# Optimization experiments

Measured on AMD Instinct MI355X. Metric: run time of the kernel, lower is better.

## Reference

```python
import jax, jax.numpy as jnp
import numpy as np

EMBED = 256
HID = EMBED * 4
NUM_EXPERTS = 4
WINDOW = 16
B, T = 4, 4096
EPS = 1e-5


def _ln(x, g, b):
    m = jnp.mean(x, axis=-1, keepdims=True)
    v = jnp.mean(jnp.square(x - m), axis=-1, keepdims=True)
    return (x - m) / jnp.sqrt(v + EPS) * g + b


def setup_inputs() -> dict:
    key = jax.random.key(0)
    ks = jax.random.split(key, 16)
    s = 0.02
    d = {
        'x': jax.random.normal(ks[0], (B, T, EMBED), jnp.float32),
        'ln1_g': jnp.ones((EMBED,), jnp.float32),
        'ln1_b': jnp.zeros((EMBED,), jnp.float32),
        'qkv_w': jax.random.normal(ks[1], (EMBED, 3 * EMBED), jnp.float32) * s,
        'qkv_b': jnp.zeros((3 * EMBED,), jnp.float32),
        'proj_w': jax.random.normal(ks[2], (EMBED, EMBED), jnp.float32) * s,
        'proj_b': jnp.zeros((EMBED,), jnp.float32),
        'attn_gate': jnp.ones((EMBED,), jnp.float32),
        'ln2_g': jnp.ones((EMBED,), jnp.float32),
        'ln2_b': jnp.zeros((EMBED,), jnp.float32),
        'gating_w': jax.random.normal(ks[3], (EMBED, NUM_EXPERTS), jnp.float32) * s,
        'gating_b': jnp.zeros((NUM_EXPERTS,), jnp.float32),
        'e_w1': jax.random.normal(ks[4], (NUM_EXPERTS, EMBED, HID), jnp.float32) * s,
        'e_b1': jnp.zeros((NUM_EXPERTS, HID), jnp.float32),
        'e_w2': jax.random.normal(ks[5], (NUM_EXPERTS, HID, EMBED), jnp.float32) * s,
        'e_b2': jnp.zeros((NUM_EXPERTS, EMBED), jnp.float32),
    }
    return d


def reference(x, ln1_g, ln1_b, qkv_w, qkv_b, proj_w, proj_b, attn_gate,
              ln2_g, ln2_b, gating_w, gating_b, e_w1, e_b1, e_w2, e_b2):
    Bx, Tx, C = x.shape
    # --- sparse attention branch ---
    h = _ln(x, ln1_g, ln1_b)
    qkv = h @ qkv_w + qkv_b                      # [B,T,3C]
    q, k, v = jnp.split(qkv, 3, axis=-1)
    scores = jnp.einsum('btc,bsc->bts', q, k) / jnp.sqrt(jnp.float32(C))
    idx = jnp.arange(Tx)
    diff = idx[:, None] - idx[None, :]           # i - j
    in_window = (diff >= 0) & (diff <= WINDOW)
    # faithful to torch code: scores outside the window (but causal) stay 0,
    # positions above the diagonal become -inf; softmax over full row
    scores = jnp.where(in_window, scores, 0.0)
    scores = jnp.where(diff >= 0, scores, -jnp.inf)
    att = jax.nn.softmax(scores, axis=-1)        # [B,T,T]
    a_out = jnp.einsum('bts,bsc->btc', att, v) * attn_gate
    x = x + a_out @ proj_w + proj_b
    # --- dense all-expert MoE branch ---
    h2 = _ln(x, ln2_g, ln2_b)
    gates = jax.nn.softmax(h2 @ gating_w + gating_b, axis=-1)     # [B,T,E]
    hid = jax.nn.gelu(jnp.einsum('btc,ech->bteh', h2, e_w1) + e_b1,
                      approximate=False)                           # [B,T,E,H]
    eo = jnp.einsum('bteh,eho->bteo', hid, e_w2) + e_b2            # [B,T,E,C]
    moe_out = jnp.einsum('bte,bteo->bto', gates, eo)
    return x + moe_out
```

## Files before the change

kernel.cpp:

```cpp
#include <hip/hip_runtime.h>
#include <hip/hip_bf16.h>
#include <math.h>

#define T_   4096
#define B_   4
#define C_   256
#define C3_  768
#define H_   1024
#define E_   4
#define M_   (B_*T_)
#define NCH_ 64
#define CHL_ (T_/NCH_)
#define KH_  4096

typedef __attribute__((ext_vector_type(8))) short short8;
typedef __attribute__((ext_vector_type(4))) float floatx4;

__device__ __forceinline__ float b2f(unsigned short u) {
  union { unsigned int i; float f; } x; x.i = ((unsigned int)u) << 16; return x.f;
}
__device__ __forceinline__ unsigned short f2b(float f) {
  __hip_bfloat16 h = __float2bfloat16(f);
  return *reinterpret_cast<unsigned short*>(&h);
}
__device__ __forceinline__ void unpack8(uint4 a, float* f) {
  unsigned int w[4] = {a.x, a.y, a.z, a.w};
  #pragma unroll
  for (int i = 0; i < 4; i++) {
    union { unsigned int u; float g; } lo, hi;
    lo.u = w[i] << 16; hi.u = w[i] & 0xffff0000u;
    f[2*i] = lo.g; f[2*i+1] = hi.g;
  }
}
__device__ __forceinline__ void gl_lds16(const void* g, void* l) {
  __builtin_amdgcn_global_load_lds(
      (const __attribute__((address_space(1))) void*)g,
      (__attribute__((address_space(3))) void*)l, 16, 0, 0);
}
__device__ __forceinline__ float gelu_s(float v) {
  float e = __expf(-1.702f * v);
  return v * __builtin_amdgcn_rcpf(1.0f + e);
}
__device__ __forceinline__ unsigned int pk_fp8x4(float a, float b, float c, float d) {
  unsigned int v = 0;
  v = __builtin_amdgcn_cvt_pk_fp8_f32(a, b, v, false);
  v = __builtin_amdgcn_cvt_pk_fp8_f32(c, d, v, true);
  return v;
}
__device__ __forceinline__ unsigned char f2fp8(float v) {
  return (unsigned char)(__builtin_amdgcn_cvt_pk_fp8_f32(v, v, 0, false) & 0xff);
}
__device__ __forceinline__ float sel4(float4 v, int e) {
  float r = v.x;
  r = (e == 1) ? v.y : r;
  r = (e == 2) ? v.z : r;
  r = (e == 3) ? v.w : r;
  return r;
}

__global__ __launch_bounds__(256) void transpose_cvt(
    const float* __restrict__ src, unsigned short* __restrict__ dst, int K, int N,
    int dstLd, size_t dstZStride) {
  __shared__ float tile[32][33];
  src += (size_t)blockIdx.z * K * N;
  dst += (size_t)blockIdx.z * dstZStride;
  int n0 = blockIdx.x * 32, k0 = blockIdx.y * 32;
  int tx = threadIdx.x, ty = threadIdx.y;
  #pragma unroll
  for (int i = 0; i < 32; i += 8)
    tile[ty + i][tx] = src[(size_t)(k0 + ty + i) * N + n0 + tx];
  __syncthreads();
  #pragma unroll
  for (int i = 0; i < 32; i += 8)
    dst[(size_t)(n0 + ty + i) * dstLd + k0 + tx] = f2b(tile[tx][ty + i]);
}

__global__ __launch_bounds__(256) void transpose_w2_fp8(
    const float* __restrict__ src, unsigned char* __restrict__ dst) {
  __shared__ float tile[32][33];
  int e = blockIdx.z;
  src += (size_t)e * H_ * C_;
  int h0 = blockIdx.x * 32, c0 = blockIdx.y * 32;
  int tx = threadIdx.x, ty = threadIdx.y;
  #pragma unroll
  for (int i = 0; i < 32; i += 8)
    tile[ty + i][tx] = src[(size_t)(h0 + ty + i) * C_ + c0 + tx];
  __syncthreads();
  int k = e * H_ + h0 + tx;
  int chunk = k >> 6, kc = k & 63;
  #pragma unroll
  for (int i = 0; i < 32; i += 8) {
    int c = c0 + ty + i;
    int sw = ((((kc >> 4) ^ (c & 3)) << 4) | (kc & 15));
    dst[((size_t)chunk * 256 + c) * 64 + sw] = f2fp8(tile[tx][ty + i] * 256.0f);
  }
}

__global__ __launch_bounds__(256) void ln1_kernel(
    const float* __restrict__ x, const float* __restrict__ g,
    const float* __restrict__ b, unsigned short* __restrict__ h) {
  __shared__ float red[4];
  int row = blockIdx.x, tid = threadIdx.x;
  float v = x[(size_t)row * C_ + tid];
  float s = v;
  #pragma unroll
  for (int o = 32; o; o >>= 1) s += __shfl_xor(s, o);
  if ((tid & 63) == 0) red[tid >> 6] = s;
  __syncthreads();
  float mean = (red[0] + red[1] + red[2] + red[3]) * (1.0f / C_);
  __syncthreads();
  float d = v - mean;
  float q = d * d;
  #pragma unroll
  for (int o = 32; o; o >>= 1) q += __shfl_xor(q, o);
  if ((tid & 63) == 0) red[tid >> 6] = q;
  __syncthreads();
  float var = (red[0] + red[1] + red[2] + red[3]) * (1.0f / C_);
  h[(size_t)row * C_ + tid] = f2b(d * rsqrtf(var + 1e-5f) * g[tid] + b[tid]);
}

__global__ __launch_bounds__(256) void ln2_gates_kernel(
    const float* __restrict__ x1, const float* __restrict__ g,
    const float* __restrict__ b, const float* __restrict__ gw,
    const float* __restrict__ gb, unsigned short* __restrict__ h2,
    float* __restrict__ gates) {
  __shared__ float red[4];
  __shared__ float redg[4][4];
  int row = blockIdx.x, tid = threadIdx.x;
  float v = x1[(size_t)row * C_ + tid];
  float s = v;
  #pragma unroll
  for (int o = 32; o; o >>= 1) s += __shfl_xor(s, o);
  if ((tid & 63) == 0) red[tid >> 6] = s;
  __syncthreads();
  float mean = (red[0] + red[1] + red[2] + red[3]) * (1.0f / C_);
  __syncthreads();
  float d = v - mean;
  float q = d * d;
  #pragma unroll
  for (int o = 32; o; o >>= 1) q += __shfl_xor(q, o);
  if ((tid & 63) == 0) red[tid >> 6] = q;
  __syncthreads();
  float var = (red[0] + red[1] + red[2] + red[3]) * (1.0f / C_);
  float hv = d * rsqrtf(var + 1e-5f) * g[tid] + b[tid];
  h2[(size_t)row * C_ + tid] = f2b(hv);
  float p0 = hv * gw[tid * 4 + 0];
  float p1 = hv * gw[tid * 4 + 1];
  float p2 = hv * gw[tid * 4 + 2];
  float p3 = hv * gw[tid * 4 + 3];
  #pragma unroll
  for (int o = 32; o; o >>= 1) {
    p0 += __shfl_xor(p0, o); p1 += __shfl_xor(p1, o);
    p2 += __shfl_xor(p2, o); p3 += __shfl_xor(p3, o);
  }
  if ((tid & 63) == 0) {
    int w = tid >> 6;
    redg[w][0] = p0; redg[w][1] = p1; redg[w][2] = p2; redg[w][3] = p3;
  }
  __syncthreads();
  if (tid == 0) {
    float t4[4];
    #pragma unroll
    for (int e = 0; e < 4; e++)
      t4[e] = redg[0][e] + redg[1][e] + redg[2][e] + redg[3][e] + gb[e];
    float m = fmaxf(fmaxf(t4[0], t4[1]), fmaxf(t4[2], t4[3]));
    float zs = 0.f;
    #pragma unroll
    for (int e = 0; e < 4; e++) { t4[e] = __expf(t4[e] - m); zs += t4[e]; }
    float inv = 1.0f / zs;
    #pragma unroll
    for (int e = 0; e < 4; e++) gates[(size_t)row * 4 + e] = t4[e] * inv;
  }
}

__global__ __launch_bounds__(256) void scan1_kernel(const unsigned short* __restrict__ qkv,
                                                    float* __restrict__ S) {
  int b = blockIdx.x >> 6, ch = blockIdx.x & 63, c = threadIdx.x;
  float s = 0.f;
  size_t base = ((size_t)b * T_ + (size_t)ch * CHL_) * C3_ + 512 + c;
  for (int t = 0; t < CHL_; t++) s += b2f(qkv[base + (size_t)t * C3_]);
  S[((size_t)b * NCH_ + ch) * C_ + c] = s;
}
__global__ __launch_bounds__(256) void scan2_kernel(float* __restrict__ S) {
  int b = blockIdx.x, c = threadIdx.x;
  float run = 0.f;
  for (int ch = 0; ch < NCH_; ch++) {
    size_t i = ((size_t)b * NCH_ + ch) * C_ + c;
    float t = S[i]; S[i] = run; run += t;
  }
}
__global__ __launch_bounds__(256) void scan3_kernel(const unsigned short* __restrict__ qkv,
                                                    const float* __restrict__ S,
                                                    unsigned short* __restrict__ Pb) {
  int b = blockIdx.x >> 6, ch = blockIdx.x & 63, c = threadIdx.x;
  float run = S[((size_t)b * NCH_ + ch) * C_ + c];
  size_t row0 = (size_t)b * T_ + (size_t)ch * CHL_;
  for (int t = 0; t < CHL_; t++) {
    run += b2f(qkv[(row0 + t) * C3_ + 512 + c]);
    Pb[(row0 + t) * C_ + c] = f2b(run);
  }
}

__global__ __launch_bounds__(256) void attn_kernel(
    const unsigned short* __restrict__ qkv, const unsigned short* __restrict__ Pb,
    const float* __restrict__ gate, unsigned short* __restrict__ aout) {
  int wave = threadIdx.x >> 6, lane = threadIdx.x & 63;
  int r = blockIdx.x * 4 + wave;
  int t = r & (T_ - 1);
  int g = lane >> 4, u = lane & 15;
  const unsigned short* qp = qkv + (size_t)r * C3_ + (u << 4);
  float qv[16];
  unpack8(*(const uint4*)qp, qv);
  unpack8(*(const uint4*)(qp + 8), qv + 8);
  float sc[5];
  #pragma unroll
  for (int rnd = 0; rnd < 5; rnd++) {
    int j = rnd * 4 + g;
    int jj = t - 16 + j;
    bool valid = (j <= 16) && (jj >= 0);
    float d = 0.f;
    if (valid) {
      const unsigned short* kp = qkv + (size_t)(r - 16 + j) * C3_ + 256 + (u << 4);
      float kv[16];
      unpack8(*(const uint4*)kp, kv);
      unpack8(*(const uint4*)(kp + 8), kv + 8);
      #pragma unroll
      for (int c = 0; c < 16; c++) d += qv[c] * kv[c];
    }
    d += __shfl_xor(d, 1); d += __shfl_xor(d, 2);
    d += __shfl_xor(d, 4); d += __shfl_xor(d, 8);
    sc[rnd] = valid ? d * 0.0625f : -1e30f;
  }
  float m = fmaxf(fmaxf(fmaxf(sc[0], sc[1]), fmaxf(sc[2], sc[3])), sc[4]);
  m = fmaxf(m, __shfl_xor(m, 16));
  m = fmaxf(m, __shfl_xor(m, 32));
  if (t > 16) m = fmaxf(m, 0.0f);
  float ev[5], Zp = 0.f;
  #pragma unroll
  for (int rnd = 0; rnd < 5; rnd++) {
    ev[rnd] = (sc[rnd] > -1e29f) ? __expf(sc[rnd] - m) : 0.f;
    Zp += ev[rnd];
  }
  Zp += __shfl_xor(Zp, 16);
  Zp += __shfl_xor(Zp, 32);
  float e0v = 0.f;
  if (t > 16) { e0v = __expf(-m); Zp += e0v * (float)(t - 16); }
  float vp[16];
  #pragma unroll
  for (int c = 0; c < 16; c++) vp[c] = 0.f;
  #pragma unroll
  for (int rnd = 0; rnd < 5; rnd++) {
    if (ev[rnd] != 0.f) {
      int j = rnd * 4 + g;
      const unsigned short* vpp = qkv + (size_t)(r - 16 + j) * C3_ + 512 + (u << 4);
      float vv[16];
      unpack8(*(const uint4*)vpp, vv);
      unpack8(*(const uint4*)(vpp + 8), vv + 8);
      #pragma unroll
      for (int c = 0; c < 16; c++) vp[c] += ev[rnd] * vv[c];
    }
  }
  #pragma unroll
  for (int c = 0; c < 16; c++) {
    vp[c] += __shfl_xor(vp[c], 16);
    vp[c] += __shfl_xor(vp[c], 32);
  }
  if (g == 0) {
    if (t > 16) {
      const unsigned short* pp = Pb + (size_t)(r - 17) * C_ + (u << 4);
      float pv[16];
      unpack8(*(const uint4*)pp, pv);
      unpack8(*(const uint4*)(pp + 8), pv + 8);
      #pragma unroll
      for (int c = 0; c < 16; c++) vp[c] += e0v * pv[c];
    }
    float inv = 1.0f / Zp;
    const float* gp = gate + (u << 4);
    unsigned int ow[8];
    #pragma unroll
    for (int i = 0; i < 8; i++) {
      unsigned short lo = f2b(vp[2*i] * inv * gp[2*i]);
      unsigned short hi = f2b(vp[2*i+1] * inv * gp[2*i+1]);
      ow[i] = (unsigned int)lo | ((unsigned int)hi << 16);
    }
    uint4 s0 = {ow[0], ow[1], ow[2], ow[3]};
    uint4 s1 = {ow[4], ow[5], ow[6], ow[7]};
    *(uint4*)(aout + (size_t)r * C_ + (u << 4)) = s0;
    *(uint4*)(aout + (size_t)r * C_ + (u << 4) + 8) = s1;
  }
}

template<int EPI>
__global__ __launch_bounds__(256) void gemm128(
    const unsigned short* __restrict__ A, const unsigned short* __restrict__ Bt,
    const float* __restrict__ bias, int K, int ldOut,
    const float* __restrict__ resid, float* __restrict__ outf,
    unsigned short* __restrict__ outb) {
  __shared__ __align__(16) unsigned short As[128 * 64];
  __shared__ __align__(16) unsigned short Bs[128 * 64];
  const int tid = threadIdx.x;
  const int wave = tid >> 6, lane = tid & 63;
  const int mBlk = blockIdx.x * 128, nBlk = blockIdx.y * 128;
  const int wm = (wave >> 1) * 64, wn = (wave & 1) * 64;
  const int lm = lane & 15, lk = (lane >> 4) * 8;
  floatx4 acc[4][4];
  #pragma unroll
  for (int i = 0; i < 4; i++)
    #pragma unroll
    for (int j = 0; j < 4; j++) acc[i][j] = (floatx4){0.f, 0.f, 0.f, 0.f};

  for (int kt = 0; kt < K; kt += 64) {
    __syncthreads();
    #pragma unroll
    for (int i = 0; i < 4; i++) {
      int seg = i * 256 + tid;
      int row = seg >> 3, g = seg & 7;
      int gc = (g ^ (row & 7)) << 3;
      gl_lds16(A + (size_t)(mBlk + row) * K + kt + gc, &As[seg * 8]);
      gl_lds16(Bt + (size_t)(nBlk + row) * K + kt + gc, &Bs[seg * 8]);
    }
    __syncthreads();
    #pragma unroll
    for (int kk = 0; kk < 64; kk += 32) {
      short8 mf[4], nf[4];
      #pragma unroll
      for (int j = 0; j < 4; j++) {
        int row = wm + j * 16 + lm;
        mf[j] = *(const short8*)&As[row * 64 + ((((kk + lk) >> 3) ^ (row & 7)) << 3)];
      }
      #pragma unroll
      for (int i = 0; i < 4; i++) {
        int row = wn + i * 16 + lm;
        nf[i] = *(const short8*)&Bs[row * 64 + ((((kk + lk) >> 3) ^ (row & 7)) << 3)];
      }
      #pragma unroll
      for (int i = 0; i < 4; i++)
        #pragma unroll
        for (int j = 0; j < 4; j++)
          acc[i][j] = __builtin_amdgcn_mfma_f32_16x16x32_bf16(nf[i], mf[j], acc[i][j], 0, 0, 0);
    }
  }
  const int lc = lane & 15, quad = lane >> 4, q4 = quad * 4;
  #pragma unroll
  for (int i = 0; i < 4; i++) {
    int n0 = nBlk + wn + i * 16 + q4;
    float4 bs = *(const float4*)&bias[n0];
    #pragma unroll
    for (int j = 0; j < 4; j++) {
      int m = mBlk + wm + j * 16 + lc;
      float v0 = acc[i][j][0] + bs.x, v1 = acc[i][j][1] + bs.y;
      float v2 = acc[i][j][2] + bs.z, v3 = acc[i][j][3] + bs.w;
      if (EPI == 0) {
        ushort4 o = {f2b(v0), f2b(v1), f2b(v2), f2b(v3)};
        *(ushort4*)&outb[(size_t)m * ldOut + n0] = o;
      } else {
        size_t idx = (size_t)m * ldOut + n0;
        float4 r = *(const float4*)&resid[idx];
        float4 o = {v0 + r.x, v1 + r.y, v2 + r.z, v3 + r.w};
        *(float4*)&outf[idx] = o;
      }
    }
  }
}

__global__ __launch_bounds__(512, 2) void moe_fused(
    const unsigned short* __restrict__ h2,
    const unsigned short* __restrict__ w1t,
    const float* __restrict__ b1,
    const unsigned char* __restrict__ w2b,
    const float* __restrict__ b2,
    const float* __restrict__ gates,
    const float* __restrict__ x1,
    float* __restrict__ out) {
  __shared__ __align__(16) unsigned short W1s[2][64 * 256];
  __shared__ __align__(16) unsigned char  W2s[2][256 * 64];
  __shared__ __align__(16) unsigned char  Hs[2][64 * 64];
  __shared__ __align__(16) float          B1s[2][64];
  const int tid = threadIdx.x;
  const int wave = tid >> 6, lane = tid & 63;
  const int lm = lane & 15, quad = lane >> 4;
  const int mb = blockIdx.x * 64;
  const bool isUp = wave < 4;
  const int uw = wave & 3;
  const int wmu = (uw >> 1) * 32;
  const int whu = (uw & 1) * 32;
  const int wc  = uw * 64;

  auto stageW1 = [&](int c, int buf) {
    const unsigned short* ws = w1t + (size_t)c * 64 * C_;
    #pragma unroll
    for (int t = 0; t < 4; t++) {
      int seg = t * 512 + tid;
      int row = seg >> 5, g = seg & 31;
      int gp = (g & 24) | ((g & 7) ^ (row & 7));
      gl_lds16(ws + (size_t)row * C_ + gp * 8, &W1s[buf][seg * 8]);
    }
    if (lane < 16)
      gl_lds16(b1 + (size_t)c * 64 + lane * 4, &B1s[buf][0]);
  };
  auto stageW2 = [&](int c, int buf) {
    const unsigned char* vs = w2b + (size_t)c * 256 * 64;
    #pragma unroll
    for (int t = 0; t < 2; t++) {
      int seg = t * 512 + tid;
      gl_lds16(vs + (size_t)seg * 16, &W2s[buf][seg * 16]);
    }
  };

  stageW1(0, 0);

  short8 af[8][2];
  float4 ga[2];
  if (isUp) {
    #pragma unroll
    for (int kk = 0; kk < 8; kk++) {
      int kc = kk * 4 + quad;
      #pragma unroll
      for (int j = 0; j < 2; j++) {
        int row = mb + wmu + j * 16 + lm;
        af[kk][j] = *(const short8*)(h2 + (size_t)row * C_ + kc * 8);
      }
    }
    #pragma unroll
    for (int j = 0; j < 2; j++)
      ga[j] = *(const float4*)(gates + (size_t)(mb + wmu + j * 16 + lm) * 4);
  }

  floatx4 dacc[4][4];
  #pragma unroll
  for (int i = 0; i < 4; i++)
    #pragma unroll
    for (int j = 0; j < 4; j++) dacc[i][j] = (floatx4){0.f, 0.f, 0.f, 0.f};

  for (int c = 0; c < 64; c++) {
    const int wb = c & 1;
    __builtin_amdgcn_s_barrier();
    __builtin_amdgcn_sched_barrier(0);
    stageW1((c + 1) & 63, wb ^ 1);
    stageW2(c, wb);
    asm volatile("s_waitcnt vmcnt(7)" ::: "memory");
    __builtin_amdgcn_s_barrier();
    __builtin_amdgcn_sched_barrier(0);

    if (isUp) {
      floatx4 uacc[2][2];
      #pragma unroll
      for (int i = 0; i < 2; i++)
        #pragma unroll
        for (int j = 0; j < 2; j++) uacc[i][j] = (floatx4){0.f, 0.f, 0.f, 0.f};
      #pragma unroll
      for (int kk = 0; kk < 8; kk++) {
        int kc = kk * 4 + quad;
        short8 nf[2];
        #pragma unroll
        for (int i = 0; i < 2; i++) {
          int row = whu + i * 16 + lm;
          nf[i] = *(const short8*)&W1s[wb][row * 256 + ((kc ^ (row & 7)) << 3)];
        }
        #pragma unroll
        for (int i = 0; i < 2; i++)
          #pragma unroll
          for (int j = 0; j < 2; j++)
            uacc[i][j] = __builtin_amdgcn_mfma_f32_16x16x32_bf16(nf[i], af[kk][j], uacc[i][j], 0, 0, 0);
      }
      int e = c >> 4;
      float gs0 = 64.0f * sel4(ga[0], e);
      float gs1 = 64.0f * sel4(ga[1], e);
      #pragma unroll
      for (int i = 0; i < 2; i++) {
        float4 bb = *(const float4*)&B1s[wb][whu + i * 16 + quad * 4];
        #pragma unroll
        for (int j = 0; j < 2; j++) {
          float gs = j ? gs1 : gs0;
          unsigned int w = pk_fp8x4(gs * gelu_s(uacc[i][j][0] + bb.x),
                                    gs * gelu_s(uacc[i][j][1] + bb.y),
                                    gs * gelu_s(uacc[i][j][2] + bb.z),
                                    gs * gelu_s(uacc[i][j][3] + bb.w));
          int m = wmu + j * 16 + lm;
          int hh = whu + i * 16 + quad * 4;
          *(unsigned int*)&Hs[wb][m * 64 + ((((hh >> 3) ^ (m & 7)) << 3) | (hh & 7))] = w;
        }
      }
      asm volatile("s_waitcnt lgkmcnt(0)" ::: "memory");
    } else if (c > 0) {
      const int pb = wb ^ 1;
      #pragma unroll
      for (int kk = 0; kk < 2; kk++) {
        long mfh[4], nfw[4];
        #pragma unroll
        for (int j = 0; j < 4; j++) {
          int m = j * 16 + lm;
          int g8 = quad + 4 * kk;
          mfh[j] = *(const long*)&Hs[pb][m * 64 + ((g8 ^ (m & 7)) << 3)];
        }
        #pragma unroll
        for (int i = 0; i < 4; i++) {
          int cr = wc + i * 16 + lm;
          int sl = ((quad >> 1) + 2 * kk) ^ (cr & 3);
          nfw[i] = *(const long*)&W2s[pb][cr * 64 + (sl << 4) + ((quad & 1) << 3)];
        }
        #pragma unroll
        for (int i = 0; i < 4; i++)
          #pragma unroll
          for (int j = 0; j < 4; j++)
            dacc[i][j] = __builtin_amdgcn_mfma_f32_16x16x32_fp8_fp8(nfw[i], mfh[j], dacc[i][j], 0, 0, 0);
      }
    }
  }

  asm volatile("s_waitcnt vmcnt(0)" ::: "memory");
  __builtin_amdgcn_s_barrier();
  __builtin_amdgcn_sched_barrier(0);
  if (!isUp) {
    #pragma unroll
    for (int kk = 0; kk < 2; kk++) {
      long mfh[4], nfw[4];
      #pragma unroll
      for (int j = 0; j < 4; j++) {
        int m = j * 16 + lm;
        int g8 = quad + 4 * kk;
        mfh[j] = *(const long*)&Hs[1][m * 64 + ((g8 ^ (m & 7)) << 3)];
      }
      #pragma unroll
      for (int i = 0; i < 4; i++) {
        int cr = wc + i * 16 + lm;
        int sl = ((quad >> 1) + 2 * kk) ^ (cr & 3);
        nfw[i] = *(const long*)&W2s[1][cr * 64 + (sl << 4) + ((quad & 1) << 3)];
      }
      #pragma unroll
      for (int i = 0; i < 4; i++)
        #pragma unroll
        for (int j = 0; j < 4; j++)
          dacc[i][j] = __builtin_amdgcn_mfma_f32_16x16x32_fp8_fp8(nfw[i], mfh[j], dacc[i][j], 0, 0, 0);
    }
    const float sc = 1.0f / 16384.0f;
    const int q4 = quad * 4;
    #pragma unroll
    for (int j = 0; j < 4; j++) {
      int m = mb + j * 16 + lm;
      float4 g4 = *(const float4*)(gates + (size_t)m * 4);
      #pragma unroll
      for (int i = 0; i < 4; i++) {
        int n0 = wc + i * 16 + q4;
        float4 bA = *(const float4*)&b2[0 * C_ + n0];
        float4 bB = *(const float4*)&b2[1 * C_ + n0];
        float4 bC = *(const float4*)&b2[2 * C_ + n0];
        float4 bD = *(const float4*)&b2[3 * C_ + n0];
        size_t idx = (size_t)m * C_ + n0;
        float4 r = *(const float4*)&x1[idx];
        float4 o;
        o.x = dacc[i][j][0]*sc + r.x + g4.x*bA.x + g4.y*bB.x + g4.z*bC.x + g4.w*bD.x;
        o.y = dacc[i][j][1]*sc + r.y + g4.x*bA.y + g4.y*bB.y + g4.z*bC.y + g4.w*bD.y;
        o.z = dacc[i][j][2]*sc + r.z + g4.x*bA.z + g4.y*bB.z + g4.z*bC.z + g4.w*bD.z;
        o.w = dacc[i][j][3]*sc + r.w + g4.x*bA.w + g4.y*bB.w + g4.z*bC.w + g4.w*bD.w;
        *(float4*)&out[idx] = o;
      }
    }
  }
}

extern "C" void kernel_launch(void* const* d_in, const int* in_sizes, int n_in,
                              void* d_out, int out_size, void* d_ws, size_t ws_size,
                              hipStream_t stream) {
  const float* x       = (const float*)d_in[0];
  const float* ln1_g   = (const float*)d_in[1];
  const float* ln1_b   = (const float*)d_in[2];
  const float* qkv_w   = (const float*)d_in[3];
  const float* qkv_b   = (const float*)d_in[4];
  const float* proj_w  = (const float*)d_in[5];
  const float* proj_b  = (const float*)d_in[6];
  const float* attn_g  = (const float*)d_in[7];
  const float* ln2_g   = (const float*)d_in[8];
  const float* ln2_b   = (const float*)d_in[9];
  const float* gat_w   = (const float*)d_in[10];
  const float* gat_b   = (const float*)d_in[11];
  const float* e_w1    = (const float*)d_in[12];
  const float* e_b1    = (const float*)d_in[13];
  const float* e_w2    = (const float*)d_in[14];
  const float* e_b2    = (const float*)d_in[15];
  float* out = (float*)d_out;

  char* p = (char*)d_ws;
  unsigned short* h    = (unsigned short*)p; p += (size_t)M_ * C_ * 2;
  unsigned short* qkv  = (unsigned short*)p; p += (size_t)M_ * C3_ * 2;
  unsigned short* Pb   = (unsigned short*)p; p += (size_t)M_ * C_ * 2;
  unsigned short* aout = (unsigned short*)p; p += (size_t)M_ * C_ * 2;
  float*          x1   = (float*)p;          p += (size_t)M_ * C_ * 4;
  unsigned short* h2   = (unsigned short*)p; p += (size_t)M_ * C_ * 2;
  float*          gts  = (float*)p;          p += (size_t)M_ * E_ * 4;
  float*          S    = (float*)p;          p += (size_t)B_ * NCH_ * C_ * 4;
  unsigned short* wq   = (unsigned short*)p; p += (size_t)C3_ * C_ * 2;
  unsigned short* wp   = (unsigned short*)p; p += (size_t)C_ * C_ * 2;
  unsigned short* w1t  = (unsigned short*)p; p += (size_t)KH_ * C_ * 2;
  unsigned char*  w2f8 = (unsigned char*)p;  p += (size_t)C_ * KH_;

  dim3 t32x8(32, 8);
  transpose_cvt<<<dim3(C3_/32, C_/32, 1), t32x8, 0, stream>>>(qkv_w, wq, C_, C3_, C_, 0);
  transpose_cvt<<<dim3(C_/32, C_/32, 1),  t32x8, 0, stream>>>(proj_w, wp, C_, C_, C_, 0);
  transpose_cvt<<<dim3(H_/32, C_/32, E_), t32x8, 0, stream>>>(e_w1, w1t, C_, H_, C_, (size_t)H_ * C_);
  transpose_w2_fp8<<<dim3(H_/32, C_/32, E_), t32x8, 0, stream>>>(e_w2, w2f8);

  ln1_kernel<<<M_, 256, 0, stream>>>(x, ln1_g, ln1_b, h);
  gemm128<0><<<dim3(M_/128, C3_/128), 256, 0, stream>>>(h, wq, qkv_b, C_, C3_,
      nullptr, nullptr, qkv);
  scan1_kernel<<<B_*NCH_, 256, 0, stream>>>(qkv, S);
  scan2_kernel<<<B_, 256, 0, stream>>>(S);
  scan3_kernel<<<B_*NCH_, 256, 0, stream>>>(qkv, S, Pb);
  attn_kernel<<<M_/4, 256, 0, stream>>>(qkv, Pb, attn_g, aout);
  gemm128<1><<<dim3(M_/128, C_/128), 256, 0, stream>>>(aout, wp, proj_b, C_, C_,
      x, x1, nullptr);
  ln2_gates_kernel<<<M_, 256, 0, stream>>>(x1, ln2_g, ln2_b, gat_w, gat_b, h2, gts);
  moe_fused<<<M_/64, 512, 0, stream>>>(h2, w1t, e_b1, w2f8, e_b2, gts, x1, out);
}
```

Before: 320.4 us.

## Double MoE block to 1024 threads and re-split up/down waves, reswizzle W2

The fused MoE kernel now runs 16 waves per block instead of 8. The up-projection work is split across 8 waves, each producing a 16-wide hidden slice for 32 rows, and the down-projection across 8 waves, each holding a 64x32 output tile. Staging loads are redistributed over the larger thread count. The fp8 W2 layout swizzle now uses (c>>1)&3, presumably to reduce LDS bank conflicts under the new access pattern. This raises per-CU parallelism and cuts per-wave accumulator registers, but adds barrier participants and makes the 4-blocks-per-CU launch bound very tight on registers and LDS.

```diff
diff --git a/kernel.cpp b/kernel.cpp
--- a/kernel.cpp
+++ b/kernel.cpp
@@ -91,7 +91,7 @@
   #pragma unroll
   for (int i = 0; i < 32; i += 8) {
     int c = c0 + ty + i;
-    int sw = ((((kc >> 4) ^ (c & 3)) << 4) | (kc & 15));
+    int sw = ((((kc >> 4) ^ ((c >> 1) & 3)) << 4) | (kc & 15));
     dst[((size_t)chunk * 256 + c) * 64 + sw] = f2fp8(tile[tx][ty + i] * 256.0f);
   }
 }
@@ -363,7 +363,7 @@
   }
 }
 
-__global__ __launch_bounds__(512, 2) void moe_fused(
+__global__ __launch_bounds__(1024, 4) void moe_fused(
     const unsigned short* __restrict__ h2,
     const unsigned short* __restrict__ w1t,
     const float* __restrict__ b1,
@@ -380,17 +380,18 @@
   const int wave = tid >> 6, lane = tid & 63;
   const int lm = lane & 15, quad = lane >> 4;
   const int mb = blockIdx.x * 64;
-  const bool isUp = wave < 4;
-  const int uw = wave & 3;
-  const int wmu = (uw >> 1) * 32;
-  const int whu = (uw & 1) * 32;
-  const int wc  = uw * 64;
+  const bool isUp = wave < 8;
+  const int rw = wave & 7;
+  const int whu = (rw & 3) * 16;
+  const int wmu = (rw >> 2) * 32;
+  const int dwc = (rw & 3) * 64;
+  const int dwm = (rw >> 2) * 32;
 
   auto stageW1 = [&](int c, int buf) {
     const unsigned short* ws = w1t + (size_t)c * 64 * C_;
     #pragma unroll
-    for (int t = 0; t < 4; t++) {
-      int seg = t * 512 + tid;
+    for (int t = 0; t < 2; t++) {
+      int seg = t * 1024 + tid;
       int row = seg >> 5, g = seg & 31;
       int gp = (g & 24) | ((g & 7) ^ (row & 7));
       gl_lds16(ws + (size_t)row * C_ + gp * 8, &W1s[buf][seg * 8]);
@@ -400,11 +401,7 @@
   };
   auto stageW2 = [&](int c, int buf) {
     const unsigned char* vs = w2b + (size_t)c * 256 * 64;
-    #pragma unroll
-    for (int t = 0; t < 2; t++) {
-      int seg = t * 512 + tid;
-      gl_lds16(vs + (size_t)seg * 16, &W2s[buf][seg * 16]);
-    }
+    gl_lds16(vs + (size_t)tid * 16, &W2s[buf][tid * 16]);
   };
 
   stageW1(0, 0);
@@ -426,11 +423,11 @@
       ga[j] = *(const float4*)(gates + (size_t)(mb + wmu + j * 16 + lm) * 4);
   }
 
-  floatx4 dacc[4][4];
+  floatx4 dacc[4][2];
   #pragma unroll
   for (int i = 0; i < 4; i++)
     #pragma unroll
-    for (int j = 0; j < 4; j++) dacc[i][j] = (floatx4){0.f, 0.f, 0.f, 0.f};
+    for (int j = 0; j < 2; j++) dacc[i][j] = (floatx4){0.f, 0.f, 0.f, 0.f};
 
   for (int c = 0; c < 64; c++) {
     const int wb = c & 1;
@@ -438,71 +435,58 @@
     __builtin_amdgcn_sched_barrier(0);
     stageW1((c + 1) & 63, wb ^ 1);
     stageW2(c, wb);
-    asm volatile("s_waitcnt vmcnt(7)" ::: "memory");
+    asm volatile("s_waitcnt vmcnt(4)" ::: "memory");
     __builtin_amdgcn_s_barrier();
     __builtin_amdgcn_sched_barrier(0);
 
     if (isUp) {
-      floatx4 uacc[2][2];
-      #pragma unroll
-      for (int i = 0; i < 2; i++)
-        #pragma unroll
-        for (int j = 0; j < 2; j++) uacc[i][j] = (floatx4){0.f, 0.f, 0.f, 0.f};
+      floatx4 uacc[2];
+      uacc[0] = (floatx4){0.f, 0.f, 0.f, 0.f};
+      uacc[1] = (floatx4){0.f, 0.f, 0.f, 0.f};
       #pragma unroll
       for (int kk = 0; kk < 8; kk++) {
         int kc = kk * 4 + quad;
-        short8 nf[2];
+        int row = whu + lm;
+        short8 nf = *(const short8*)&W1s[wb][row * 256 + ((kc ^ (row & 7)) << 3)];
         #pragma unroll
-        for (int i = 0; i < 2; i++) {
-          int row = whu + i * 16 + lm;
-          nf[i] = *(const short8*)&W1s[wb][row * 256 + ((kc ^ (row & 7)) << 3)];
-        }
-        #pragma unroll
-        for (int i = 0; i < 2; i++)
-          #pragma unroll
-          for (int j = 0; j < 2; j++)
-            uacc[i][j] = __builtin_amdgcn_mfma_f32_16x16x32_bf16(nf[i], af[kk][j], uacc[i][j], 0, 0, 0);
+        for (int j = 0; j < 2; j++)
+          uacc[j] = __builtin_amdgcn_mfma_f32_16x16x32_bf16(nf, af[kk][j], uacc[j], 0, 0, 0);
       }
       int e = c >> 4;
-      float gs0 = 64.0f * sel4(ga[0], e);
-      float gs1 = 64.0f * sel4(ga[1], e);
-      #pragma unroll
-      for (int i = 0; i < 2; i++) {
-        float4 bb = *(const float4*)&B1s[wb][whu + i * 16 + quad * 4];
-        #pragma unroll
-        for (int j = 0; j < 2; j++) {
-          float gs = j ? gs1 : gs0;
-          unsigned int w = pk_fp8x4(gs * gelu_s(uacc[i][j][0] + bb.x),
-                                    gs * gelu_s(uacc[i][j][1] + bb.y),
-                                    gs * gelu_s(uacc[i][j][2] + bb.z),
-                                    gs * gelu_s(uacc[i][j][3] + bb.w));
-          int m = wmu + j * 16 + lm;
-          int hh = whu + i * 16 + quad * 4;
-          *(unsigned int*)&Hs[wb][m * 64 + ((((hh >> 3) ^ (m & 7)) << 3) | (hh & 7))] = w;
-        }
+      float4 bb = *(const float4*)&B1s[wb][whu + quad * 4];
+      #pragma unroll
+      for (int j = 0; j < 2; j++) {
+        float gs = 64.0f * sel4(ga[j], e);
+        unsigned int w = pk_fp8x4(gs * gelu_s(uacc[j][0] + bb.x),
+                                  gs * gelu_s(uacc[j][1] + bb.y),
+                                  gs * gelu_s(uacc[j][2] + bb.z),
+                                  gs * gelu_s(uacc[j][3] + bb.w));
+        int m = wmu + j * 16 + lm;
+        int hh = whu + quad * 4;
+        *(unsigned int*)&Hs[wb][m * 64 + ((((hh >> 3) ^ (m & 7)) << 3) | (hh & 7))] = w;
       }
       asm volatile("s_waitcnt lgkmcnt(0)" ::: "memory");
     } else if (c > 0) {
       const int pb = wb ^ 1;
       #pragma unroll
       for (int kk = 0; kk < 2; kk++) {
-        long mfh[4], nfw[4];
+        long mfh[2], nfw[4];
         #pragma unroll
-        for (int j = 0; j < 4; j++) {
-          int m = j * 16 + lm;
+        for (int j = 0; j < 2; j++) {
+          int m = dwm + j * 16 + lm;
           int g8 = quad + 4 * kk;
           mfh[j] = *(const long*)&Hs[pb][m * 64 + ((g8 ^ (m & 7)) << 3)];
         }
         #pragma unroll
         for (int i = 0; i < 4; i++) {
-          int cr = wc + i * 16 + lm;
-          int sl = ((quad >> 1) + 2 * kk) ^ (cr & 3);
+          int cr = dwc + i * 16 + lm;
+          int sl = ((quad >> 1) + 2 * kk) ^ ((cr >> 1) & 3);
           nfw[i] = *(const long*)&W2s[pb][cr * 64 + (sl << 4) + ((quad & 1) << 3)];
         }
         #pragma unroll
         for (int i = 0; i < 4; i++)
           #pragma unroll
-          for (int j = 0; j < 4; j++)
+          for (int j = 0; j < 2; j++)
             dacc[i][j] = __builtin_amdgcn_mfma_f32_16x16x32_fp8_fp8(nfw[i], mfh[j], dacc[i][j], 0, 0, 0);
       }
     }
@@ -514,34 +498,34 @@
   if (!isUp) {
     #pragma unroll
     for (int kk = 0; kk < 2; kk++) {
-      long mfh[4], nfw[4];
-      #pragma unroll
-      for (int j = 0; j < 4; j++) {
-        int m = j * 16 + lm;
+      long mfh[2], nfw[4];
+      #pragma unroll
+      for (int j = 0; j < 2; j++) {
+        int m = dwm + j * 16 + lm;
         int g8 = quad + 4 * kk;
         mfh[j] = *(const long*)&Hs[1][m * 64 + ((g8 ^ (m & 7)) << 3)];
       }
       #pragma unroll
       for (int i = 0; i < 4; i++) {
-        int cr = wc + i * 16 + lm;
-        int sl = ((quad >> 1) + 2 * kk) ^ (cr & 3);
+        int cr = dwc + i * 16 + lm;
+        int sl = ((quad >> 1) + 2 * kk) ^ ((cr >> 1) & 3);
         nfw[i] = *(const long*)&W2s[1][cr * 64 + (sl << 4) + ((quad & 1) << 3)];
       }
       #pragma unroll
       for (int i = 0; i < 4; i++)
         #pragma unroll
-        for (int j = 0; j < 4; j++)
+        for (int j = 0; j < 2; j++)
           dacc[i][j] = __builtin_amdgcn_mfma_f32_16x16x32_fp8_fp8(nfw[i], mfh[j], dacc[i][j], 0, 0, 0);
     }
     const float sc = 1.0f / 16384.0f;
     const int q4 = quad * 4;
     #pragma unroll
-    for (int j = 0; j < 4; j++) {
-      int m = mb + j * 16 + lm;
+    for (int j = 0; j < 2; j++) {
+      int m = mb + dwm + j * 16 + lm;
       float4 g4 = *(const float4*)(gates + (size_t)m * 4);
       #pragma unroll
       for (int i = 0; i < 4; i++) {
-        int n0 = wc + i * 16 + q4;
+        int n0 = dwc + i * 16 + q4;
         float4 bA = *(const float4*)&b2[0 * C_ + n0];
         float4 bB = *(const float4*)&b2[1 * C_ + n0];
         float4 bC = *(const float4*)&b2[2 * C_ + n0];
@@ -610,5 +594,5 @@
   gemm128<1><<<dim3(M_/128, C_/128), 256, 0, stream>>>(aout, wp, proj_b, C_, C_,
       x, x1, nullptr);
   ln2_gates_kernel<<<M_, 256, 0, stream>>>(x1, ln2_g, ln2_b, gat_w, gat_b, h2, gts);
-  moe_fused<<<M_/64, 512, 0, stream>>>(h2, w1t, e_b1, w2f8, e_b2, gts, x1, out);
-}
+  moe_fused<<<M_/64, 1024, 0, stream>>>(h2, w1t, e_b1, w2f8, e_b2, gts, x1, out);
+}
```

Result: slower. 398.6 us (+24.4%).
